# Optimization experiments

Measured on AMD Instinct MI355X. Metric: run time of the kernel, lower is better.

The kernel has to match this reference:

```python
import jax, jax.numpy as jnp
import numpy as np

B, N, E, H = 8, 512, 256, 8
HD = E // H
FF = 4 * E
TOPK = max(1, int(N * 0.2))
FW_MAX_DIST = 10      # default of get_shortest_path_matrix
EMB_MAX_IDX = 6       # spd encoder: max_dist(5) + 1
LN_EPS = 1e-5


def _layernorm(x, g, b):
    m = jnp.mean(x, axis=-1, keepdims=True)
    v = jnp.var(x, axis=-1, keepdims=True)
    return (x - m) / jnp.sqrt(v + LN_EPS) * g + b


def setup_inputs() -> dict:
    key = jax.random.key(0)
    ks = jax.random.split(key, 12)
    s = 0.02
    return {
        "x": jax.random.normal(ks[0], (B, N, E), jnp.float32),
        "adj": jax.random.uniform(ks[1], (B, N, N), jnp.float32),
        "emb_spd": (jax.random.normal(ks[2], (EMB_MAX_IDX + 1, H), jnp.float32) * s),
        "w_qkv": jax.random.normal(ks[3], (3 * E, E), jnp.float32) * s,
        "b_qkv": jnp.zeros((3 * E,), jnp.float32),
        "w_out": jax.random.normal(ks[4], (E, E), jnp.float32) * s,
        "b_out": jnp.zeros((E,), jnp.float32),
        "w_ff1": jax.random.normal(ks[5], (FF, E), jnp.float32) * s,
        "b_ff1": jnp.zeros((FF,), jnp.float32),
        "w_ff2": jax.random.normal(ks[6], (E, FF), jnp.float32) * s,
        "b_ff2": jnp.zeros((E,), jnp.float32),
        "g1": jnp.ones((E,), jnp.float32),
        "beta1": jnp.zeros((E,), jnp.float32),
        "g2": jnp.ones((E,), jnp.float32),
        "beta2": jnp.zeros((E,), jnp.float32),
        "w_pool": jax.random.normal(ks[7], (1, E), jnp.float32) * s,
        "b_pool": jnp.zeros((1,), jnp.float32),
    }


def _combined_mask(adj, emb_spd):
    # top-k per row -> binary adjacency via scatter
    _, idx = jax.lax.top_k(adj, TOPK)                       # [B,N,k]
    bi = jnp.arange(B)[:, None, None]
    ri = jnp.arange(N)[None, :, None]
    binary = jnp.zeros_like(adj).at[bi, ri, idx].set(1.0)   # [B,N,N]

    # Floyd-Warshall shortest paths
    dist = jnp.where(binary == 1.0, 1.0, jnp.inf)
    ids = jnp.arange(N)
    dist = dist.at[:, ids, ids].set(0.0)

    def body(k, d):
        return jnp.minimum(d, d[:, :, k][:, :, None] + d[:, k, :][:, None, :])

    dist = jax.lax.fori_loop(0, N, body, dist)
    dist_i = jnp.where(dist > FW_MAX_DIST, -1.0, dist).astype(jnp.int32)

    # spatial bias embedding: indices = clamp(dist+1, 0, max_dist+1)
    sp_idx = jnp.clip(dist_i + 1, 0, EMB_MAX_IDX)           # [B,N,N]
    bias = jnp.transpose(emb_spd[sp_idx], (0, 3, 1, 2))     # [B,H,N,N]

    base = jnp.where(binary == 0.0, -jnp.inf, 0.0)[:, None] # [B,1,N,N]
    return base + bias                                      # [B,H,N,N]


def reference(x, adj, emb_spd, w_qkv, b_qkv, w_out, b_out,
              w_ff1, b_ff1, w_ff2, b_ff2, g1, beta1, g2, beta2,
              w_pool, b_pool):
    mask = _combined_mask(adj, emb_spd)                     # [B,H,N,N]

    # multi-head self-attention (PyTorch MHA, post-norm encoder layer, eval)
    qkv = x @ w_qkv.T + b_qkv                               # [B,N,3E]
    q, k, v = jnp.split(qkv, 3, axis=-1)
    q = q.reshape(B, N, H, HD).transpose(0, 2, 1, 3)
    k = k.reshape(B, N, H, HD).transpose(0, 2, 1, 3)
    v = v.reshape(B, N, H, HD).transpose(0, 2, 1, 3)
    scores = jnp.einsum("bhqd,bhkd->bhqk", q, k) / np.sqrt(HD) + mask
    attn = jax.nn.softmax(scores, axis=-1)
    ctx = jnp.einsum("bhqk,bhkd->bhqd", attn, v)
    ctx = ctx.transpose(0, 2, 1, 3).reshape(B, N, E)
    attn_out = ctx @ w_out.T + b_out

    x1 = _layernorm(x + attn_out, g1, beta1)
    ff = jax.nn.relu(x1 @ w_ff1.T + b_ff1) @ w_ff2.T + b_ff2
    x2 = _layernorm(x1 + ff, g2, beta2)

    # attention pooling over nodes
    w = jax.nn.softmax(jnp.tanh(x2 @ w_pool.T + b_pool), axis=1)  # [B,N,1]
    return jnp.sum(x2 * w, axis=1)                          # [B,E]
```

## Files before the change

### kernel.cpp

```cpp
#include <hip/hip_runtime.h>
#include <math.h>


#define B_ 8
#define N_ 512
#define E_ 256
#define H_ 8
#define HD_ 32
#define TOPK_ 102

typedef __attribute__((ext_vector_type(8))) short bf16x8;
typedef __attribute__((ext_vector_type(4))) float f32x4;

__device__ __forceinline__ unsigned short f2b(float f) {
  unsigned u = __builtin_bit_cast(unsigned, f);
  return (unsigned short)((u + 0x7FFFu + ((u >> 16) & 1u)) >> 16);
}

__global__ __launch_bounds__(256) void cvt_all(
    const float* __restrict__ x, const float* __restrict__ wqkv,
    const float* __restrict__ wout, const float* __restrict__ wff1,
    const float* __restrict__ wff2, unsigned short* __restrict__ xb,
    unsigned short* __restrict__ wqkvb, unsigned short* __restrict__ woutb,
    unsigned short* __restrict__ wff1b, unsigned short* __restrict__ wff2b) {
  int i = (blockIdx.x * 256 + threadIdx.x) * 4;
  const float* src;
  unsigned short* dst;
  int off;
  if (i < 1048576)      { src = x;    dst = xb;    off = i; }
  else if (i < 1245184) { src = wqkv; dst = wqkvb; off = i - 1048576; }
  else if (i < 1310720) { src = wout; dst = woutb; off = i - 1245184; }
  else if (i < 1572864) { src = wff1; dst = wff1b; off = i - 1310720; }
  else                  { src = wff2; dst = wff2b; off = i - 1572864; }
  float4 v = *(const float4*)(src + off);
  ushort4 o;
  o.x = f2b(v.x); o.y = f2b(v.y); o.z = f2b(v.z); o.w = f2b(v.w);
  *(ushort4*)(dst + off) = o;
}

__global__ __launch_bounds__(256) void topk_kernel(const float* __restrict__ adj,
                                                   unsigned int* __restrict__ bits) {
  const int row = blockIdx.x;
  const float* a = adj + (size_t)row * N_;
  __shared__ unsigned int hist[1024];
  __shared__ float cval[N_];
  __shared__ int cidx[N_];
  __shared__ int s_cnt;
  __shared__ int s_bb;
  __shared__ int s_need;
  __shared__ unsigned int rowbits[16];
  __shared__ int wsum[4];
  const int t = threadIdx.x;
  const int lane = t & 63;
  const int wave = t >> 6;

  hist[t] = 0u; hist[t + 256] = 0u; hist[t + 512] = 0u; hist[t + 768] = 0u;
  if (t == 0) s_cnt = 0;
  float v0 = a[t];
  float v1 = a[t + 256];
  __syncthreads();
  const int b0 = min(1023, max(0, (int)(v0 * 1024.0f)));
  const int b1 = min(1023, max(0, (int)(v1 * 1024.0f)));
  atomicAdd(&hist[b0], 1u);
  atomicAdd(&hist[b1], 1u);
  __syncthreads();
  const int base = 1020 - 4 * t;
  const int h0 = (int)hist[base], h1 = (int)hist[base + 1];
  const int h2 = (int)hist[base + 2], h3 = (int)hist[base + 3];
  const int g = h0 + h1 + h2 + h3;
  int sc = g;
  #pragma unroll
  for (int off = 1; off < 64; off <<= 1) {
    int y = __shfl_up(sc, off);
    sc += (lane >= off) ? y : 0;
  }
  if (lane == 63) wsum[wave] = sc;
  __syncthreads();
  int wo = 0;
  for (int w = 0; w < wave; w++) wo += wsum[w];
  const int incl = sc + wo;
  const int excl = incl - g;
  if (excl < TOPK_ && incl >= TOPK_) {
    int cum = excl;
    int bb = base;
    const int hh[4] = {h3, h2, h1, h0};
    const int bs[4] = {base + 3, base + 2, base + 1, base};
    #pragma unroll
    for (int u = 0; u < 4; u++) {
      if (cum + hh[u] >= TOPK_) { bb = bs[u]; break; }
      cum += hh[u];
    }
    s_bb = bb;
    s_need = TOPK_ - cum;
  }
  __syncthreads();
  const int bb = s_bb;
  const int need = s_need;
  const bool sel0 = (b0 > bb);
  const bool sel1 = (b1 > bb);
  if (b0 == bb) { int p = atomicAdd(&s_cnt, 1); cval[p] = v0; cidx[p] = t; }
  if (b1 == bb) { int p = atomicAdd(&s_cnt, 1); cval[p] = v1; cidx[p] = t + 256; }
  unsigned long long m0 = __ballot(sel0);
  unsigned long long m1 = __ballot(sel1);
  if (lane == 0) {
    rowbits[2 * wave + 0] = (unsigned int)m0;
    rowbits[2 * wave + 1] = (unsigned int)(m0 >> 32);
    rowbits[8 + 2 * wave + 0] = (unsigned int)m1;
    rowbits[8 + 2 * wave + 1] = (unsigned int)(m1 >> 32);
  }
  __syncthreads();
  const int cnt = s_cnt;
  for (int c = t; c < cnt; c += 256) {
    const float v = cval[c];
    const int idx = cidx[c];
    int r = 0;
    for (int j = 0; j < cnt; j++) {
      const float vj = cval[j];
      const int ij = cidx[j];
      if (vj > v || (vj == v && ij < idx)) r++;
    }
    if (r < need) atomicOr(&rowbits[idx >> 5], 1u << (idx & 31));
  }
  __syncthreads();
  if (t < 16) bits[(size_t)row * 16 + t] = rowbits[t];
}

__global__ __launch_bounds__(256) void gemm_mfma(
    const unsigned short* __restrict__ A, const unsigned short* __restrict__ W,
    const float* __restrict__ bias, const float* __restrict__ res,
    void* __restrict__ Cout, unsigned short* __restrict__ kG,
    unsigned short* __restrict__ vG, int M, int N, int K, int flags) {
  __shared__ __align__(16) unsigned short Af[8 * 64 * 8];
  __shared__ __align__(16) unsigned short Wf[8 * 64 * 8];
  const int tid = threadIdx.x;
  const int m0 = blockIdx.y * 64, n0 = blockIdx.x * 64;
  const int wave = tid >> 6, lane = tid & 63;
  const int wm = wave & 1, wn = wave >> 1;
  const int q = lane >> 4, l15 = lane & 15;
  const int r = tid >> 2, c0 = tid & 3;

  f32x4 acc[2][2];
  #pragma unroll
  for (int i = 0; i < 2; i++)
    #pragma unroll
    for (int j = 0; j < 2; j++) acc[i][j] = (f32x4){0.f, 0.f, 0.f, 0.f};

  const size_t arow = (size_t)(m0 + r) * K;
  const size_t wrow = (size_t)(n0 + r) * K;
  for (int k0 = 0; k0 < K; k0 += 64) {
    uint4 a0 = *(const uint4*)(A + arow + k0 + c0 * 8);
    uint4 a1 = *(const uint4*)(A + arow + k0 + (c0 + 4) * 8);
    uint4 w0 = *(const uint4*)(W + wrow + k0 + c0 * 8);
    uint4 w1 = *(const uint4*)(W + wrow + k0 + (c0 + 4) * 8);
    __syncthreads();
    {
      int kc = c0 >> 2, qq = c0 & 3;
      int s0 = ((r >> 4) * 2 + kc) * 64 + (r & 15) + qq * 16;
      int kc1 = (c0 + 4) >> 2, qq1 = (c0 + 4) & 3;
      int s1 = ((r >> 4) * 2 + kc1) * 64 + (r & 15) + qq1 * 16;
      *(uint4*)(Af + s0 * 8) = a0;
      *(uint4*)(Af + s1 * 8) = a1;
      *(uint4*)(Wf + s0 * 8) = w0;
      *(uint4*)(Wf + s1 * 8) = w1;
    }
    __syncthreads();
    #pragma unroll
    for (int kc = 0; kc < 2; kc++) {
      bf16x8 af[2], wf[2];
      #pragma unroll
      for (int mt = 0; mt < 2; mt++)
        af[mt] = *(const bf16x8*)(Af + (((wm * 2 + mt) * 2 + kc) * 64 + lane) * 8);
      #pragma unroll
      for (int nt = 0; nt < 2; nt++)
        wf[nt] = *(const bf16x8*)(Wf + (((wn * 2 + nt) * 2 + kc) * 64 + lane) * 8);
      #pragma unroll
      for (int mt = 0; mt < 2; mt++)
        #pragma unroll
        for (int nt = 0; nt < 2; nt++)
          acc[mt][nt] = __builtin_amdgcn_mfma_f32_16x16x32_bf16(af[mt], wf[nt], acc[mt][nt], 0, 0, 0);
    }
  }
  #pragma unroll
  for (int nt = 0; nt < 2; nt++) {
    const int col = n0 + (wn * 2 + nt) * 16 + l15;
    const float bv = bias[col];
    #pragma unroll
    for (int mt = 0; mt < 2; mt++) {
      const int rowb = m0 + (wm * 2 + mt) * 16 + q * 4;
      float ov[4];
      #pragma unroll
      for (int reg = 0; reg < 4; reg++) {
        float o = acc[mt][nt][reg] + bv;
        if (res) o += res[(size_t)(rowb + reg) * N + col];
        if (flags & 1) o = fmaxf(o, 0.f);
        ov[reg] = o;
      }
      if (kG && col >= 256 && col < 512) {
        const int dfull = col - 256;
        const int hh2 = dfull >> 5, d = dfull & 31;
        const int q2 = d >> 3, sub = d & 7;
        const int bidx = rowb >> 9, j = rowb & 511;
        const int jt = j >> 6, jtile = (j >> 4) & 3, jl = j & 15;
        unsigned short* kp = kG +
            ((size_t)(((bidx * 8 + hh2) * 8 + jt) * 4 + jtile) * 64 + q2 * 16 + jl) * 8 + sub;
        kp[0] = f2b(ov[0]); kp[8] = f2b(ov[1]); kp[16] = f2b(ov[2]); kp[24] = f2b(ov[3]);
      } else if (vG && col >= 512) {
        const int dfull = col - 512;
        const int hh2 = dfull >> 5, d = dfull & 31;
        const int dt = d >> 4, dl = d & 15;
        const int bidx = rowb >> 9, j = rowb & 511;
        const int jt = j >> 6, jj = j & 63;
        const int kc = jj >> 5, q2 = (jj >> 3) & 3, sub0 = jj & 7;
        ushort4 st;
        st.x = f2b(ov[0]); st.y = f2b(ov[1]); st.z = f2b(ov[2]); st.w = f2b(ov[3]);
        *(ushort4*)(vG +
            ((size_t)(((bidx * 8 + hh2) * 8 + jt) * 4 + dt * 2 + kc) * 64 + q2 * 16 + dl) * 8 + sub0) = st;
      } else {
        #pragma unroll
        for (int reg = 0; reg < 4; reg++) {
          if (flags & 2) ((unsigned short*)Cout)[(size_t)(rowb + reg) * N + col] = f2b(ov[reg]);
          else           ((float*)Cout)[(size_t)(rowb + reg) * N + col] = ov[reg];
        }
      }
    }
  }
}

__global__ __launch_bounds__(256) void attn_mfma(
    const unsigned short* __restrict__ qkv, const unsigned short* __restrict__ kG,
    const unsigned short* __restrict__ vG, const unsigned int* __restrict__ bits,
    const float* __restrict__ emb, unsigned short* __restrict__ ctxo) {
  const int bx = blockIdx.x;
  const int ib = bx & 7;
  const int h = (bx >> 3) & 7;
  const int b = bx >> 6;
  const int tid = threadIdx.x;
  const int lane = tid & 63;
  const int wave = tid >> 6;
  const int q = lane >> 4, l15 = lane & 15;

  __shared__ __align__(16) unsigned int mrow[64 * 16];
  __shared__ __align__(16) unsigned short pF[4][2 * 64 * 8];

  {
    int rr = tid >> 2, wq = tid & 3;
    uint4 mw = *(const uint4*)(bits + ((size_t)(b * N_ + ib * 64 + rr)) * 16 + wq * 4);
    *(uint4*)(mrow + rr * 16 + wq * 4) = mw;
  }
  __syncthreads();

  const int i0w = ib * 64 + wave * 16;
  const bf16x8 qf = *(const bf16x8*)(qkv + ((size_t)(b * N_ + i0w + l15)) * 768 + h * HD_ + q * 8);
  const float delta = emb[1 * H_ + h] - emb[2 * H_ + h];
  const float scale = 0.17677669529663687f;

  float m_run[4], l_run[4];
  #pragma unroll
  for (int e = 0; e < 4; e++) { m_run[e] = -1e30f; l_run[e] = 0.f; }
  f32x4 cacc[2];
  cacc[0] = (f32x4){0.f, 0.f, 0.f, 0.f};
  cacc[1] = (f32x4){0.f, 0.f, 0.f, 0.f};

  unsigned short* pbase = &pF[wave][0];
  const unsigned short* kb = kG + (size_t)(b * 8 + h) * 8 * 4 * 512;
  const unsigned short* vb = vG + (size_t)(b * 8 + h) * 8 * 4 * 512;

  #pragma unroll 1
  for (int jt = 0; jt < 8; jt++) {
    f32x4 s4[4];
    #pragma unroll
    for (int jtile = 0; jtile < 4; jtile++) {
      bf16x8 kf = *(const bf16x8*)(kb + (size_t)(jt * 4 + jtile) * 512 + lane * 8);
      s4[jtile] = __builtin_amdgcn_mfma_f32_16x16x32_bf16(qf, kf, (f32x4){0.f, 0.f, 0.f, 0.f}, 0, 0, 0);
    }
    unsigned long long mw64[4];
    #pragma unroll
    for (int reg = 0; reg < 4; reg++)
      mw64[reg] = *(const unsigned long long*)(mrow + (wave * 16 + q * 4 + reg) * 16 + jt * 2);
    float smat[4][4];
    #pragma unroll
    for (int jtile = 0; jtile < 4; jtile++) {
      #pragma unroll
      for (int reg = 0; reg < 4; reg++) {
        unsigned int w = (jtile & 2) ? (unsigned int)(mw64[reg] >> 32) : (unsigned int)mw64[reg];
        bool allowed = ((w >> ((jtile & 1) * 16 + l15)) & 1u) != 0u;
        int ig = ib * 64 + wave * 16 + q * 4 + reg;
        int jg = jt * 64 + jtile * 16 + l15;
        float s = s4[jtile][reg] * scale + ((jg == ig) ? delta : 0.f);
        smat[jtile][reg] = allowed ? s : -INFINITY;
      }
    }
    float alpha[4], pmat[4][4];
    #pragma unroll
    for (int reg = 0; reg < 4; reg++) {
      float mloc = fmaxf(fmaxf(smat[0][reg], smat[1][reg]), fmaxf(smat[2][reg], smat[3][reg]));
      #pragma unroll
      for (int off = 1; off < 16; off <<= 1) mloc = fmaxf(mloc, __shfl_xor(mloc, off));
      float mnew = fmaxf(m_run[reg], mloc);
      alpha[reg] = __expf(m_run[reg] - mnew);
      m_run[reg] = mnew;
      float ps = 0.f;
      #pragma unroll
      for (int jtile = 0; jtile < 4; jtile++) {
        float p = __expf(smat[jtile][reg] - mnew);
        pmat[jtile][reg] = p;
        ps += p;
      }
      #pragma unroll
      for (int off = 1; off < 16; off <<= 1) ps += __shfl_xor(ps, off);
      l_run[reg] = l_run[reg] * alpha[reg] + ps;
      cacc[0][reg] *= alpha[reg];
      cacc[1][reg] *= alpha[reg];
    }
    #pragma unroll
    for (int jtile = 0; jtile < 4; jtile++) {
      int j_l = jtile * 16 + l15;
      int sl = ((j_l >> 5) * 64 + ((j_l >> 3) & 3) * 16) * 8 + (j_l & 7);
      #pragma unroll
      for (int reg = 0; reg < 4; reg++)
        pbase[sl + (q * 4 + reg) * 8] = f2b(pmat[jtile][reg]);
    }
    #pragma unroll
    for (int kc = 0; kc < 2; kc++) {
      bf16x8 pf = *(const bf16x8*)(pbase + (kc * 64 + lane) * 8);
      #pragma unroll
      for (int dt = 0; dt < 2; dt++) {
        bf16x8 vf = *(const bf16x8*)(vb + (size_t)(jt * 4 + dt * 2 + kc) * 512 + lane * 8);
        cacc[dt] = __builtin_amdgcn_mfma_f32_16x16x32_bf16(pf, vf, cacc[dt], 0, 0, 0);
      }
    }
  }
  #pragma unroll
  for (int reg = 0; reg < 4; reg++) {
    const float linv = 1.f / l_run[reg];
    const size_t row = (size_t)(b * N_ + i0w + q * 4 + reg);
    #pragma unroll
    for (int dt = 0; dt < 2; dt++)
      ctxo[row * E_ + h * HD_ + dt * 16 + l15] = f2b(cacc[dt][reg] * linv);
  }
}

__global__ __launch_bounds__(256) void layernorm_kernel(
    const float* __restrict__ t, const float* __restrict__ g,
    const float* __restrict__ be, float* __restrict__ out,
    unsigned short* __restrict__ outb, const float* __restrict__ wp,
    const float* __restrict__ bp, float* __restrict__ ew) {
  const int row = blockIdx.x;
  const int tid = threadIdx.x;
  float v = t[(size_t)row * E_ + tid];
  float s = v, s2 = v * v;
  #pragma unroll
  for (int off = 32; off > 0; off >>= 1) {
    s += __shfl_xor(s, off);
    s2 += __shfl_xor(s2, off);
  }
  __shared__ float sh[8];
  const int wave = tid >> 6, lane = tid & 63;
  if (lane == 0) { sh[wave] = s; sh[4 + wave] = s2; }
  __syncthreads();
  s = sh[0] + sh[1] + sh[2] + sh[3];
  s2 = sh[4] + sh[5] + sh[6] + sh[7];
  float mean = s * (1.f / 256.f);
  float var = s2 * (1.f / 256.f) - mean * mean;
  float inv = rsqrtf(var + 1e-5f);
  float o = (v - mean) * inv * g[tid] + be[tid];
  out[(size_t)row * E_ + tid] = o;
  if (outb) outb[(size_t)row * E_ + tid] = f2b(o);
  if (ew) {
    float d = o * wp[tid];
    #pragma unroll
    for (int off = 32; off > 0; off >>= 1) d += __shfl_xor(d, off);
    __syncthreads();
    if (lane == 0) sh[wave] = d;
    __syncthreads();
    if (tid == 0) {
      float dot = sh[0] + sh[1] + sh[2] + sh[3] + bp[0];
      ew[row] = __expf(tanhf(dot));
    }
  }
}

__global__ __launch_bounds__(256) void pool_partial(
    const float* __restrict__ x2, const float* __restrict__ ew,
    float* __restrict__ partial, float* __restrict__ pwsum) {
  const int c = blockIdx.x;
  const int b = blockIdx.y;
  const int tid = threadIdx.x;
  const int r0 = b * N_ + c * 16;
  float acc = 0.f;
  #pragma unroll
  for (int n = 0; n < 16; n++)
    acc += ew[r0 + n] * x2[(size_t)(r0 + n) * E_ + tid];
  partial[(size_t)(b * 32 + c) * E_ + tid] = acc;
  if (tid < 16) {
    float w = ew[r0 + tid];
    #pragma unroll
    for (int off = 1; off < 16; off <<= 1) w += __shfl_xor(w, off);
    if (tid == 0) pwsum[b * 32 + c] = w;
  }
}

__global__ __launch_bounds__(256) void pool_final(
    const float* __restrict__ partial, const float* __restrict__ pwsum,
    float* __restrict__ out) {
  const int b = blockIdx.x;
  const int tid = threadIdx.x;
  float acc = 0.f, ws = 0.f;
  #pragma unroll
  for (int c = 0; c < 32; c++) acc += partial[(size_t)(b * 32 + c) * E_ + tid];
  #pragma unroll
  for (int c = 0; c < 32; c++) ws += pwsum[b * 32 + c];
  out[b * E_ + tid] = acc / ws;
}

extern "C" void kernel_launch(void* const* d_in, const int* in_sizes, int n_in,
                              void* d_out, int out_size, void* d_ws, size_t ws_size,
                              hipStream_t stream) {
  (void)in_sizes; (void)n_in; (void)out_size; (void)ws_size;
  const float* x      = (const float*)d_in[0];
  const float* adj    = (const float*)d_in[1];
  const float* emb    = (const float*)d_in[2];
  const float* w_qkv  = (const float*)d_in[3];
  const float* b_qkv  = (const float*)d_in[4];
  const float* w_out  = (const float*)d_in[5];
  const float* b_out  = (const float*)d_in[6];
  const float* w_ff1  = (const float*)d_in[7];
  const float* b_ff1  = (const float*)d_in[8];
  const float* w_ff2  = (const float*)d_in[9];
  const float* b_ff2  = (const float*)d_in[10];
  const float* g1     = (const float*)d_in[11];
  const float* be1    = (const float*)d_in[12];
  const float* g2     = (const float*)d_in[13];
  const float* be2    = (const float*)d_in[14];
  const float* w_pool = (const float*)d_in[15];
  const float* b_pool = (const float*)d_in[16];

  char* ws = (char*)d_ws;
  unsigned int*   bits  = (unsigned int*)ws;
  unsigned short* xb    = (unsigned short*)(ws + 262144);
  unsigned short* qkvb  = (unsigned short*)(ws + 2359296);
  unsigned short* hffb  = xb;
  unsigned short* ctxb  = (unsigned short*)(ws + 8650752);
  unsigned short* x1b   = (unsigned short*)(ws + 10747904);
  unsigned short* wqkvb = (unsigned short*)(ws + 12845056);
  unsigned short* woutb = (unsigned short*)(ws + 13238272);
  unsigned short* wff1b = (unsigned short*)(ws + 13369344);
  unsigned short* wff2b = (unsigned short*)(ws + 13893632);
  unsigned short* vG    = (unsigned short*)(ws + 14417920);
  unsigned short* kG    = (unsigned short*)(ws + 16515072);
  float*          tbuf  = (float*)(ws + 18612224);
  float*          x1    = (float*)(ws + 22806528);
  float*          x2    = (float*)(ws + 27000832);
  float*          ew      = (float*)(ws + 8650752);
  float*          partial = (float*)(ws + 8650752 + 16384);
  float*          pwsum   = (float*)(ws + 8650752 + 16384 + 262144);
  float*          outp  = (float*)d_out;

  const int M = B_ * N_;

  cvt_all<<<1835008 / 1024, 256, 0, stream>>>(x, w_qkv, w_out, w_ff1, w_ff2,
                                              xb, wqkvb, woutb, wff1b, wff2b);
  topk_kernel<<<B_ * N_, 256, 0, stream>>>(adj, bits);
  gemm_mfma<<<dim3(768 / 64, M / 64), 256, 0, stream>>>(
      xb, wqkvb, b_qkv, nullptr, qkvb, kG, vG, M, 768, E_, 2);
  attn_mfma<<<B_ * H_ * (N_ / 64), 256, 0, stream>>>(qkvb, kG, vG, bits, emb, ctxb);
  gemm_mfma<<<dim3(E_ / 64, M / 64), 256, 0, stream>>>(
      ctxb, woutb, b_out, x, tbuf, nullptr, nullptr, M, E_, E_, 0);
  layernorm_kernel<<<M, 256, 0, stream>>>(tbuf, g1, be1, x1, x1b,
                                          nullptr, nullptr, nullptr);
  gemm_mfma<<<dim3(1024 / 64, M / 64), 256, 0, stream>>>(
      x1b, wff1b, b_ff1, nullptr, hffb, nullptr, nullptr, M, 1024, E_, 1 | 2);
  gemm_mfma<<<dim3(E_ / 64, M / 64), 256, 0, stream>>>(
      hffb, wff2b, b_ff2, x1, tbuf, nullptr, nullptr, M, E_, 1024, 0);
  layernorm_kernel<<<M, 256, 0, stream>>>(tbuf, g2, be2, x2, nullptr,
                                          w_pool, b_pool, ew);
  pool_partial<<<dim3(32, 8), 256, 0, stream>>>(x2, ew, partial, pwsum);
  pool_final<<<B_, 256, 0, stream>>>(partial, pwsum, outp);
}
```

Before: 177.5 us.

## Fuse conversion with top-k, LN2 with pooling, and trim QKV output stores

Merges the bf16 conversion into the top-k kernel launch, has the QKV GEMM write only Q rows densely alongside the K/V tiled layouts, processes eight rows per layernorm block, and folds the second layernorm together with the attention-pooling partial sums. These cut kernel launches, redundant global writes of K/V, and the round trip of x2 through memory. The top-k tie buffer is capped at 64 candidates, which relies on few values sharing a histogram bin.

```diff
diff --git a/kernel.cpp b/kernel.cpp
--- a/kernel.cpp
+++ b/kernel.cpp
@@ -17,40 +17,39 @@
   return (unsigned short)((u + 0x7FFFu + ((u >> 16) & 1u)) >> 16);
 }
 
-__global__ __launch_bounds__(256) void cvt_all(
+__global__ __launch_bounds__(256) void cvt_topk(
+    const float* __restrict__ adj, unsigned int* __restrict__ bits,
     const float* __restrict__ x, const float* __restrict__ wqkv,
     const float* __restrict__ wout, const float* __restrict__ wff1,
     const float* __restrict__ wff2, unsigned short* __restrict__ xb,
     unsigned short* __restrict__ wqkvb, unsigned short* __restrict__ woutb,
     unsigned short* __restrict__ wff1b, unsigned short* __restrict__ wff2b) {
-  int i = (blockIdx.x * 256 + threadIdx.x) * 4;
-  const float* src;
-  unsigned short* dst;
-  int off;
-  if (i < 1048576)      { src = x;    dst = xb;    off = i; }
-  else if (i < 1245184) { src = wqkv; dst = wqkvb; off = i - 1048576; }
-  else if (i < 1310720) { src = wout; dst = woutb; off = i - 1245184; }
-  else if (i < 1572864) { src = wff1; dst = wff1b; off = i - 1310720; }
-  else                  { src = wff2; dst = wff2b; off = i - 1572864; }
-  float4 v = *(const float4*)(src + off);
-  ushort4 o;
-  o.x = f2b(v.x); o.y = f2b(v.y); o.z = f2b(v.z); o.w = f2b(v.w);
-  *(ushort4*)(dst + off) = o;
-}
-
-__global__ __launch_bounds__(256) void topk_kernel(const float* __restrict__ adj,
-                                                   unsigned int* __restrict__ bits) {
-  const int row = blockIdx.x;
-  const float* a = adj + (size_t)row * N_;
   __shared__ unsigned int hist[1024];
-  __shared__ float cval[N_];
-  __shared__ int cidx[N_];
-  __shared__ int s_cnt;
-  __shared__ int s_bb;
-  __shared__ int s_need;
+  __shared__ float cval[64];
+  __shared__ int cidx[64];
+  __shared__ int s_cnt, s_bb, s_need;
   __shared__ unsigned int rowbits[16];
   __shared__ int wsum[4];
   const int t = threadIdx.x;
+
+  if (blockIdx.x >= 4096) {
+    int i = ((blockIdx.x - 4096) * 256 + t) * 4;
+    const float* src;
+    unsigned short* dst;
+    int off;
+    if (i < 1048576)      { src = x;    dst = xb;    off = i; }
+    else if (i < 1245184) { src = wqkv; dst = wqkvb; off = i - 1048576; }
+    else if (i < 1310720) { src = wout; dst = woutb; off = i - 1245184; }
+    else if (i < 1572864) { src = wff1; dst = wff1b; off = i - 1310720; }
+    else                  { src = wff2; dst = wff2b; off = i - 1572864; }
+    float4 v = *(const float4*)(src + off);
+    ushort4 o;
+    o.x = f2b(v.x); o.y = f2b(v.y); o.z = f2b(v.z); o.w = f2b(v.w);
+    *(ushort4*)(dst + off) = o;
+    return;
+  }
+  const int row = blockIdx.x;
+  const float* a = adj + (size_t)row * N_;
   const int lane = t & 63;
   const int wave = t >> 6;
 
@@ -98,8 +97,8 @@
   const int need = s_need;
   const bool sel0 = (b0 > bb);
   const bool sel1 = (b1 > bb);
-  if (b0 == bb) { int p = atomicAdd(&s_cnt, 1); cval[p] = v0; cidx[p] = t; }
-  if (b1 == bb) { int p = atomicAdd(&s_cnt, 1); cval[p] = v1; cidx[p] = t + 256; }
+  if (b0 == bb) { int p = atomicAdd(&s_cnt, 1); if (p < 64) { cval[p] = v0; cidx[p] = t; } }
+  if (b1 == bb) { int p = atomicAdd(&s_cnt, 1); if (p < 64) { cval[p] = v1; cidx[p] = t + 256; } }
   unsigned long long m0 = __ballot(sel0);
   unsigned long long m1 = __ballot(sel1);
   if (lane == 0) {
@@ -109,7 +108,7 @@
     rowbits[8 + 2 * wave + 1] = (unsigned int)(m1 >> 32);
   }
   __syncthreads();
-  const int cnt = s_cnt;
+  const int cnt = min(s_cnt, 64);
   for (int c = t; c < cnt; c += 256) {
     const float v = cval[c];
     const int idx = cidx[c];
@@ -195,39 +194,47 @@
         if (flags & 1) o = fmaxf(o, 0.f);
         ov[reg] = o;
       }
-      if (kG && col >= 256 && col < 512) {
-        const int dfull = col - 256;
-        const int hh2 = dfull >> 5, d = dfull & 31;
-        const int q2 = d >> 3, sub = d & 7;
-        const int bidx = rowb >> 9, j = rowb & 511;
-        const int jt = j >> 6, jtile = (j >> 4) & 3, jl = j & 15;
-        unsigned short* kp = kG +
-            ((size_t)(((bidx * 8 + hh2) * 8 + jt) * 4 + jtile) * 64 + q2 * 16 + jl) * 8 + sub;
-        kp[0] = f2b(ov[0]); kp[8] = f2b(ov[1]); kp[16] = f2b(ov[2]); kp[24] = f2b(ov[3]);
-      } else if (vG && col >= 512) {
-        const int dfull = col - 512;
-        const int hh2 = dfull >> 5, d = dfull & 31;
-        const int dt = d >> 4, dl = d & 15;
-        const int bidx = rowb >> 9, j = rowb & 511;
-        const int jt = j >> 6, jj = j & 63;
-        const int kc = jj >> 5, q2 = (jj >> 3) & 3, sub0 = jj & 7;
-        ushort4 st;
-        st.x = f2b(ov[0]); st.y = f2b(ov[1]); st.z = f2b(ov[2]); st.w = f2b(ov[3]);
-        *(ushort4*)(vG +
-            ((size_t)(((bidx * 8 + hh2) * 8 + jt) * 4 + dt * 2 + kc) * 64 + q2 * 16 + dl) * 8 + sub0) = st;
+      if (flags & 4) {
+        if (col < 256) {
+          #pragma unroll
+          for (int reg = 0; reg < 4; reg++)
+            ((unsigned short*)Cout)[(size_t)(rowb + reg) * 256 + col] = f2b(ov[reg]);
+        } else if (col < 512) {
+          const int dfull = col - 256;
+          const int hh2 = dfull >> 5, d = dfull & 31;
+          const int q2 = d >> 3, sub = d & 7;
+          const int bidx = rowb >> 9, j = rowb & 511;
+          const int jt = j >> 6, jtile = (j >> 4) & 3, jl = j & 15;
+          unsigned short* kp = kG +
+              ((size_t)(((bidx * 8 + hh2) * 8 + jt) * 4 + jtile) * 64 + q2 * 16 + jl) * 8 + sub;
+          kp[0] = f2b(ov[0]); kp[8] = f2b(ov[1]); kp[16] = f2b(ov[2]); kp[24] = f2b(ov[3]);
+        } else {
+          const int dfull = col - 512;
+          const int hh2 = dfull >> 5, d = dfull & 31;
+          const int dt = d >> 4, dl = d & 15;
+          const int bidx = rowb >> 9, j = rowb & 511;
+          const int jt = j >> 6, jj = j & 63;
+          const int kc = jj >> 5, q2 = (jj >> 3) & 3, sub0 = jj & 7;
+          ushort4 st;
+          st.x = f2b(ov[0]); st.y = f2b(ov[1]); st.z = f2b(ov[2]); st.w = f2b(ov[3]);
+          *(ushort4*)(vG +
+              ((size_t)(((bidx * 8 + hh2) * 8 + jt) * 4 + dt * 2 + kc) * 64 + q2 * 16 + dl) * 8 + sub0) = st;
+        }
+      } else if (flags & 2) {
+        #pragma unroll
+        for (int reg = 0; reg < 4; reg++)
+          ((unsigned short*)Cout)[(size_t)(rowb + reg) * N + col] = f2b(ov[reg]);
       } else {
         #pragma unroll
-        for (int reg = 0; reg < 4; reg++) {
-          if (flags & 2) ((unsigned short*)Cout)[(size_t)(rowb + reg) * N + col] = f2b(ov[reg]);
-          else           ((float*)Cout)[(size_t)(rowb + reg) * N + col] = ov[reg];
-        }
+        for (int reg = 0; reg < 4; reg++)
+          ((float*)Cout)[(size_t)(rowb + reg) * N + col] = ov[reg];
       }
     }
   }
 }
 
 __global__ __launch_bounds__(256) void attn_mfma(
-    const unsigned short* __restrict__ qkv, const unsigned short* __restrict__ kG,
+    const unsigned short* __restrict__ qb, const unsigned short* __restrict__ kG,
     const unsigned short* __restrict__ vG, const unsigned int* __restrict__ bits,
     const float* __restrict__ emb, unsigned short* __restrict__ ctxo) {
   const int bx = blockIdx.x;
@@ -250,7 +257,7 @@
   __syncthreads();
 
   const int i0w = ib * 64 + wave * 16;
-  const bf16x8 qf = *(const bf16x8*)(qkv + ((size_t)(b * N_ + i0w + l15)) * 768 + h * HD_ + q * 8);
+  const bf16x8 qf = *(const bf16x8*)(qb + ((size_t)(b * N_ + i0w + l15)) * 256 + h * HD_ + q * 8);
   const float delta = emb[1 * H_ + h] - emb[2 * H_ + h];
   const float scale = 0.17677669529663687f;
 
@@ -340,64 +347,81 @@
   }
 }
 
-__global__ __launch_bounds__(256) void layernorm_kernel(
+__global__ __launch_bounds__(256) void ln8_kernel(
     const float* __restrict__ t, const float* __restrict__ g,
     const float* __restrict__ be, float* __restrict__ out,
-    unsigned short* __restrict__ outb, const float* __restrict__ wp,
-    const float* __restrict__ bp, float* __restrict__ ew) {
-  const int row = blockIdx.x;
+    unsigned short* __restrict__ outb) {
+  __shared__ float sh[8];
   const int tid = threadIdx.x;
-  float v = t[(size_t)row * E_ + tid];
-  float s = v, s2 = v * v;
-  #pragma unroll
-  for (int off = 32; off > 0; off >>= 1) {
-    s += __shfl_xor(s, off);
-    s2 += __shfl_xor(s2, off);
-  }
+  const int wave = tid >> 6, lane = tid & 63;
+  const float gv = g[tid], bev = be[tid];
+  #pragma unroll 1
+  for (int rr = 0; rr < 8; rr++) {
+    const int row = blockIdx.x * 8 + rr;
+    float v = t[(size_t)row * E_ + tid];
+    float s = v, s2 = v * v;
+    #pragma unroll
+    for (int off = 32; off > 0; off >>= 1) {
+      s += __shfl_xor(s, off);
+      s2 += __shfl_xor(s2, off);
+    }
+    __syncthreads();
+    if (lane == 0) { sh[wave] = s; sh[4 + wave] = s2; }
+    __syncthreads();
+    s = sh[0] + sh[1] + sh[2] + sh[3];
+    s2 = sh[4] + sh[5] + sh[6] + sh[7];
+    float mean = s * (1.f / 256.f);
+    float var = s2 * (1.f / 256.f) - mean * mean;
+    float inv = rsqrtf(var + 1e-5f);
+    float o = (v - mean) * inv * gv + bev;
+    out[(size_t)row * E_ + tid] = o;
+    outb[(size_t)row * E_ + tid] = f2b(o);
+  }
+}
+
+__global__ __launch_bounds__(256) void ln2pool_kernel(
+    const float* __restrict__ t, const float* __restrict__ g,
+    const float* __restrict__ be, const float* __restrict__ wp,
+    const float* __restrict__ bp, float* __restrict__ partial,
+    float* __restrict__ pwsum) {
   __shared__ float sh[8];
+  const int tid = threadIdx.x;
   const int wave = tid >> 6, lane = tid & 63;
-  if (lane == 0) { sh[wave] = s; sh[4 + wave] = s2; }
-  __syncthreads();
-  s = sh[0] + sh[1] + sh[2] + sh[3];
-  s2 = sh[4] + sh[5] + sh[6] + sh[7];
-  float mean = s * (1.f / 256.f);
-  float var = s2 * (1.f / 256.f) - mean * mean;
-  float inv = rsqrtf(var + 1e-5f);
-  float o = (v - mean) * inv * g[tid] + be[tid];
-  out[(size_t)row * E_ + tid] = o;
-  if (outb) outb[(size_t)row * E_ + tid] = f2b(o);
-  if (ew) {
-    float d = o * wp[tid];
+  const int c = blockIdx.x;
+  const float gv = g[tid], bev = be[tid], wpv = wp[tid], bpv = bp[0];
+  float pacc = 0.f, esum = 0.f;
+  #pragma unroll 1
+  for (int rr = 0; rr < 8; rr++) {
+    const int row = c * 8 + rr;
+    float v = t[(size_t)row * E_ + tid];
+    float s = v, s2 = v * v;
+    #pragma unroll
+    for (int off = 32; off > 0; off >>= 1) {
+      s += __shfl_xor(s, off);
+      s2 += __shfl_xor(s2, off);
+    }
+    __syncthreads();
+    if (lane == 0) { sh[wave] = s; sh[4 + wave] = s2; }
+    __syncthreads();
+    s = sh[0] + sh[1] + sh[2] + sh[3];
+    s2 = sh[4] + sh[5] + sh[6] + sh[7];
+    float mean = s * (1.f / 256.f);
+    float var = s2 * (1.f / 256.f) - mean * mean;
+    float inv = rsqrtf(var + 1e-5f);
+    float o = (v - mean) * inv * gv + bev;
+    float d = o * wpv;
     #pragma unroll
     for (int off = 32; off > 0; off >>= 1) d += __shfl_xor(d, off);
     __syncthreads();
     if (lane == 0) sh[wave] = d;
     __syncthreads();
-    if (tid == 0) {
-      float dot = sh[0] + sh[1] + sh[2] + sh[3] + bp[0];
-      ew[row] = __expf(tanhf(dot));
-    }
-  }
-}
-
-__global__ __launch_bounds__(256) void pool_partial(
-    const float* __restrict__ x2, const float* __restrict__ ew,
-    float* __restrict__ partial, float* __restrict__ pwsum) {
-  const int c = blockIdx.x;
-  const int b = blockIdx.y;
-  const int tid = threadIdx.x;
-  const int r0 = b * N_ + c * 16;
-  float acc = 0.f;
-  #pragma unroll
-  for (int n = 0; n < 16; n++)
-    acc += ew[r0 + n] * x2[(size_t)(r0 + n) * E_ + tid];
-  partial[(size_t)(b * 32 + c) * E_ + tid] = acc;
-  if (tid < 16) {
-    float w = ew[r0 + tid];
-    #pragma unroll
-    for (int off = 1; off < 16; off <<= 1) w += __shfl_xor(w, off);
-    if (tid == 0) pwsum[b * 32 + c] = w;
-  }
+    float dot = sh[0] + sh[1] + sh[2] + sh[3] + bpv;
+    float e = __expf(tanhf(dot));
+    pacc += e * o;
+    esum += e;
+  }
+  partial[(size_t)c * E_ + tid] = pacc;
+  if (tid == 0) pwsum[c] = esum;
 }
 
 __global__ __launch_bounds__(256) void pool_final(
@@ -407,9 +431,9 @@
   const int tid = threadIdx.x;
   float acc = 0.f, ws = 0.f;
   #pragma unroll
-  for (int c = 0; c < 32; c++) acc += partial[(size_t)(b * 32 + c) * E_ + tid];
-  #pragma unroll
-  for (int c = 0; c < 32; c++) ws += pwsum[b * 32 + c];
+  for (int c = 0; c < 64; c++) acc += partial[(size_t)(b * 64 + c) * E_ + tid];
+  #pragma unroll
+  for (int c = 0; c < 64; c++) ws += pwsum[b * 64 + c];
   out[b * E_ + tid] = acc / ws;
 }
 
@@ -438,42 +462,37 @@
   char* ws = (char*)d_ws;
   unsigned int*   bits  = (unsigned int*)ws;
   unsigned short* xb    = (unsigned short*)(ws + 262144);
-  unsigned short* qkvb  = (unsigned short*)(ws + 2359296);
-  unsigned short* hffb  = xb;
+  unsigned short* qb    = (unsigned short*)(ws + 2359296);
+  unsigned short* kG    = (unsigned short*)(ws + 4456448);
+  unsigned short* vG    = (unsigned short*)(ws + 6553600);
   unsigned short* ctxb  = (unsigned short*)(ws + 8650752);
-  unsigned short* x1b   = (unsigned short*)(ws + 10747904);
-  unsigned short* wqkvb = (unsigned short*)(ws + 12845056);
-  unsigned short* woutb = (unsigned short*)(ws + 13238272);
-  unsigned short* wff1b = (unsigned short*)(ws + 13369344);
-  unsigned short* wff2b = (unsigned short*)(ws + 13893632);
-  unsigned short* vG    = (unsigned short*)(ws + 14417920);
-  unsigned short* kG    = (unsigned short*)(ws + 16515072);
-  float*          tbuf  = (float*)(ws + 18612224);
-  float*          x1    = (float*)(ws + 22806528);
-  float*          x2    = (float*)(ws + 27000832);
-  float*          ew      = (float*)(ws + 8650752);
-  float*          partial = (float*)(ws + 8650752 + 16384);
-  float*          pwsum   = (float*)(ws + 8650752 + 16384 + 262144);
+  float*          tbuf  = (float*)(ws + 10747904);
+  float*          x1    = (float*)(ws + 14942208);
+  unsigned short* x1b   = (unsigned short*)(ws + 19136512);
+  unsigned short* hffb  = (unsigned short*)(ws + 21233664);
+  unsigned short* wqkvb = (unsigned short*)(ws + 29622272);
+  unsigned short* woutb = (unsigned short*)(ws + 30015488);
+  unsigned short* wff1b = (unsigned short*)(ws + 30146560);
+  unsigned short* wff2b = (unsigned short*)(ws + 30670848);
+  float*          partial = (float*)(ws + 31195136);
+  float*          pwsum   = (float*)(ws + 31719424);
   float*          outp  = (float*)d_out;
 
   const int M = B_ * N_;
 
-  cvt_all<<<1835008 / 1024, 256, 0, stream>>>(x, w_qkv, w_out, w_ff1, w_ff2,
-                                              xb, wqkvb, woutb, wff1b, wff2b);
-  topk_kernel<<<B_ * N_, 256, 0, stream>>>(adj, bits);
+  cvt_topk<<<4096 + 1792, 256, 0, stream>>>(adj, bits, x, w_qkv, w_out, w_ff1,
+                                            w_ff2, xb, wqkvb, woutb, wff1b, wff2b);
   gemm_mfma<<<dim3(768 / 64, M / 64), 256, 0, stream>>>(
-      xb, wqkvb, b_qkv, nullptr, qkvb, kG, vG, M, 768, E_, 2);
-  attn_mfma<<<B_ * H_ * (N_ / 64), 256, 0, stream>>>(qkvb, kG, vG, bits, emb, ctxb);
+      xb, wqkvb, b_qkv, nullptr, qb, kG, vG, M, 768, E_, 4);
+  attn_mfma<<<B_ * H_ * (N_ / 64), 256, 0, stream>>>(qb, kG, vG, bits, emb, ctxb);
   gemm_mfma<<<dim3(E_ / 64, M / 64), 256, 0, stream>>>(
       ctxb, woutb, b_out, x, tbuf, nullptr, nullptr, M, E_, E_, 0);
-  layernorm_kernel<<<M, 256, 0, stream>>>(tbuf, g1, be1, x1, x1b,
-                                          nullptr, nullptr, nullptr);
+  ln8_kernel<<<M / 8, 256, 0, stream>>>(tbuf, g1, be1, x1, x1b);
   gemm_mfma<<<dim3(1024 / 64, M / 64), 256, 0, stream>>>(
       x1b, wff1b, b_ff1, nullptr, hffb, nullptr, nullptr, M, 1024, E_, 1 | 2);
   gemm_mfma<<<dim3(E_ / 64, M / 64), 256, 0, stream>>>(
       hffb, wff2b, b_ff2, x1, tbuf, nullptr, nullptr, M, E_, 1024, 0);
-  layernorm_kernel<<<M, 256, 0, stream>>>(tbuf, g2, be2, x2, nullptr,
-                                          w_pool, b_pool, ew);
-  pool_partial<<<dim3(32, 8), 256, 0, stream>>>(x2, ew, partial, pwsum);
+  ln2pool_kernel<<<M / 8, 256, 0, stream>>>(tbuf, g2, be2, w_pool, b_pool,
+                                            partial, pwsum);
   pool_final<<<B_, 256, 0, stream>>>(partial, pwsum, outp);
 }
```

After: 178.5 us, median of 2. About the same (+0.6%).
